# Optimization experiments

Hardware: AMD Instinct MI355X
Metric: run time of the kernel (lower is better)

## Reference

```python
import jax, jax.numpy as jnp
import numpy as np

N = 50000
E = 800000
NEG_SLOPE = 0.2


def gatv2_layer(x, src, dst, Wl, Wr, att, bias, heads, ch):
    # x: [N, Fin]; Wl/Wr: [Fin, heads*ch]; att: [heads, ch]; bias: [heads*ch]
    xl = (x @ Wl).reshape(N, heads, ch)  # source transform
    xr = (x @ Wr).reshape(N, heads, ch)  # target transform
    e = xl[src] + xr[dst]                              # [E, H, C]
    s = jnp.einsum('ehc,hc->eh', jax.nn.leaky_relu(e, NEG_SLOPE), att)  # [E, H]
    # scatter-softmax over incoming edges of each target node
    smax = jax.ops.segment_max(s, dst, num_segments=N)  # [N, H]
    ex = jnp.exp(s - smax[dst])
    denom = jax.ops.segment_sum(ex, dst, num_segments=N)
    alpha = ex / denom[dst]                             # [E, H]
    out = jax.ops.segment_sum(xl[src] * alpha[..., None], dst, num_segments=N)  # [N, H, C]
    return out.reshape(N, heads * ch) + bias


def setup_inputs() -> dict:
    key = jax.random.key(0)
    ks = jax.random.split(key, 12)
    x = jax.random.normal(ks[0], (N, 128), dtype=jnp.float32)
    edge_index = jax.random.randint(ks[1], (2, E), 0, N, dtype=jnp.int64)
    edge_attr = jax.random.normal(ks[2], (E, 16), dtype=jnp.float32)
    s1 = 1.0 / np.sqrt(128.0)
    # layer 1: 128 -> 64, heads=2 (concat -> 128)
    Wl1 = jax.random.normal(ks[3], (128, 128), dtype=jnp.float32) * s1
    Wr1 = jax.random.normal(ks[4], (128, 128), dtype=jnp.float32) * s1
    att1 = jax.random.normal(ks[5], (2, 64), dtype=jnp.float32) * 0.1
    b1 = jnp.zeros((128,), dtype=jnp.float32)
    # layer 2: 128 -> 128, heads=1
    Wl2 = jax.random.normal(ks[6], (128, 128), dtype=jnp.float32) * s1
    Wr2 = jax.random.normal(ks[7], (128, 128), dtype=jnp.float32) * s1
    att2 = jax.random.normal(ks[8], (1, 128), dtype=jnp.float32) * 0.1
    b2 = jnp.zeros((128,), dtype=jnp.float32)
    return {"x": x, "edge_index": edge_index, "edge_attr": edge_attr,
            "Wl1": Wl1, "Wr1": Wr1, "att1": att1, "b1": b1,
            "Wl2": Wl2, "Wr2": Wr2, "att2": att2, "b2": b2}


def reference(x, edge_index, edge_attr, Wl1, Wr1, att1, b1, Wl2, Wr2, att2, b2):
    # using_edge_attr=False default path: edge_attr ignored.
    # GATv2Conv default add_self_loops=True
    loops = jnp.arange(N, dtype=edge_index.dtype)
    src = jnp.concatenate([edge_index[0], loops])
    dst = jnp.concatenate([edge_index[1], loops])
    h = gatv2_layer(x, src, dst, Wl1, Wr1, att1, b1, heads=2, ch=64)
    out = gatv2_layer(h, src, dst, Wl2, Wr2, att2, b2, heads=1, ch=128)
    return out
```

## Files before the change

### kernel.cpp

```cpp
#include <hip/hip_runtime.h>

#define NEG_SLOPE 0.2f
#define NPB 256
#define CHUNK 4096
#define BCAP 5120

typedef _Float16 f16x8 __attribute__((ext_vector_type(8)));
typedef _Float16 f16x4 __attribute__((ext_vector_type(4)));
typedef _Float16 f16x2 __attribute__((ext_vector_type(2)));
typedef float    f32x4 __attribute__((ext_vector_type(4)));
typedef float    f32x8 __attribute__((ext_vector_type(8)));

#if defined(__has_builtin)
#if __has_builtin(__builtin_amdgcn_fdot2)
#define HAVE_FDOT2 1
#endif
#endif

__device__ __forceinline__ f32x8 cvt8(f16x8 v) {
    return __builtin_convertvector(v, f32x8);
}

template <int CTRL>
__device__ __forceinline__ float dpp_add(float v) {
    int o = __builtin_amdgcn_update_dpp(0, __builtin_bit_cast(int, v),
                                        CTRL, 0xF, 0xF, true);
    return v + __builtin_bit_cast(float, o);
}

__global__ __launch_bounds__(256) void prep_kernel(
    const float* __restrict__ W0, const float* __restrict__ W1,
    const float* __restrict__ W2, const float* __restrict__ W3,
    _Float16* __restrict__ wt,
    const float* __restrict__ x, _Float16* __restrict__ xh,
    _Float16* __restrict__ xlo, int total, int* __restrict__ gcursor)
{
    int t = threadIdx.x;
    if (blockIdx.x < 256) {
        if (blockIdx.x == 0) gcursor[t] = t * BCAP;
        int idx = blockIdx.x * 256 + t;
        int m = idx >> 14;
        int k = (idx >> 7) & 127;
        int n = idx & 127;
        const float* W = (m == 0) ? W0 : (m == 1) ? W1 : (m == 2) ? W2 : W3;
        wt[m * 16384 + n * 128 + k] = (_Float16)W[k * 128 + n];
    } else {
        int i = (blockIdx.x - 256) * 256 + t;
        if (i * 2 < total) {
            float2 f = *(const float2*)(x + (size_t)i * 2);
            _Float16 h0 = (_Float16)f.x, h1 = (_Float16)f.y;
            _Float16 l0 = (_Float16)(f.x - (float)h0), l1 = (_Float16)(f.y - (float)h1);
            *(f16x2*)(xh  + (size_t)i * 2) = (f16x2){h0, h1};
            *(f16x2*)(xlo + (size_t)i * 2) = (f16x2){l0, l1};
        }
    }
}

__global__ __launch_bounds__(256) void gemm_f16_kernel(
    const _Float16* __restrict__ Ahi, const _Float16* __restrict__ Alo,
    const _Float16* __restrict__ Wt0, const _Float16* __restrict__ Wt1,
    _Float16* __restrict__ Cl, _Float16* __restrict__ Cr, int N)
{
    const _Float16* Wt = blockIdx.y ? Wt1 : Wt0;
    _Float16* C = blockIdx.y ? Cr : Cl;

    __shared__ _Float16 ldsW[128 * 136];

    const int tid = threadIdx.x;
    const int wave = tid >> 6;
    const int lane = tid & 63;
    const int mrow = lane & 15;
    const int quad = lane >> 4;
    const int rbase = blockIdx.x * 128 + wave * 32;

    const int sn = tid >> 1, shf = tid & 1;
    float4 stg[8];
    {
        const float4* g = (const float4*)(Wt + sn * 128 + shf * 64);
#pragma unroll
        for (int j = 0; j < 8; j++) stg[j] = g[j];
    }

    f16x8 ah[2][4], al[2][4];
#pragma unroll
    for (int rt = 0; rt < 2; rt++) {
        int r = rbase + rt * 16 + mrow;
        if (r > N - 1) r = N - 1;
        const _Float16* pa = Ahi + (size_t)r * 128 + quad * 8;
        const _Float16* pl = Alo + (size_t)r * 128 + quad * 8;
#pragma unroll
        for (int s = 0; s < 4; s++) {
            ah[rt][s] = *(const f16x8*)(pa + s * 32);
            al[rt][s] = *(const f16x8*)(pl + s * 32);
        }
    }

    {
        float4* d = (float4*)&ldsW[sn * 136 + shf * 64];
#pragma unroll
        for (int j = 0; j < 8; j++) d[j] = stg[j];
    }

    f32x4 acc[2][8];
#pragma unroll
    for (int rt = 0; rt < 2; rt++)
#pragma unroll
        for (int c = 0; c < 8; c++) acc[rt][c] = (f32x4){0.f, 0.f, 0.f, 0.f};

    __syncthreads();

#pragma unroll
    for (int s = 0; s < 4; s++) {
#pragma unroll
        for (int c = 0; c < 8; c++) {
            f16x8 bw = *(const f16x8*)&ldsW[(c * 16 + mrow) * 136 + s * 32 + quad * 8];
            acc[0][c] = __builtin_amdgcn_mfma_f32_16x16x32_f16(ah[0][s], bw, acc[0][c], 0, 0, 0);
            acc[0][c] = __builtin_amdgcn_mfma_f32_16x16x32_f16(al[0][s], bw, acc[0][c], 0, 0, 0);
            acc[1][c] = __builtin_amdgcn_mfma_f32_16x16x32_f16(ah[1][s], bw, acc[1][c], 0, 0, 0);
            acc[1][c] = __builtin_amdgcn_mfma_f32_16x16x32_f16(al[1][s], bw, acc[1][c], 0, 0, 0);
        }
    }

#pragma unroll
    for (int rt = 0; rt < 2; rt++)
#pragma unroll
        for (int i = 0; i < 4; i++) {
            int r = rbase + rt * 16 + quad * 4 + i;
            if (r < N) {
                _Float16* cr = C + (size_t)r * 128 + mrow;
#pragma unroll
                for (int c = 0; c < 8; c++) cr[c * 16] = (_Float16)acc[rt][c][i];
            }
        }
}

__global__ __launch_bounds__(256) void bucketA_kernel(
    const int* __restrict__ ei, int* __restrict__ gcursor,
    int2* __restrict__ staging, int E)
{
    __shared__ int bh[256];
    __shared__ int bbase[256];
    int t = threadIdx.x;
    bh[t] = 0;
    __syncthreads();
    int base = blockIdx.x * CHUNK;
    int srcv[16], dstv[16], rb[16];
#pragma unroll
    for (int j = 0; j < 16; j++) {
        int e = base + t + j * 256;
        if (e < E) {
            int d = ei[E + e];
            srcv[j] = ei[e];
            dstv[j] = d;
            int bk = d >> 8;
            int r = atomicAdd(&bh[bk], 1);
            rb[j] = (r << 8) | bk;
        } else rb[j] = -1;
    }
    __syncthreads();
    if (bh[t]) bbase[t] = atomicAdd(&gcursor[t], bh[t]);
    __syncthreads();
#pragma unroll
    for (int j = 0; j < 16; j++) {
        if (rb[j] >= 0) {
            int bk = rb[j] & 255, r = rb[j] >> 8;
            staging[bbase[bk] + r] = make_int2(srcv[j], dstv[j]);
        }
    }
}

__global__ __launch_bounds__(256) void passB_kernel(
    const int2* __restrict__ staging, const int* __restrict__ gcursor,
    int* __restrict__ start, int* __restrict__ deg,
    int* __restrict__ sorted_src, int N)
{
    __shared__ int lhist[256], lscan[256], lcur[256];
    int b = blockIdx.x, t = threadIdx.x;
    int r0 = b * BCAP;
    int r1 = gcursor[b];
    lhist[t] = 0;
    __syncthreads();
    for (int i = r0 + t; i < r1; i += 256) atomicAdd(&lhist[staging[i].y & 255], 1);
    __syncthreads();
    int v = lhist[t];
    lscan[t] = v;
    __syncthreads();
    for (int off = 1; off < 256; off <<= 1) {
        int u = (t >= off) ? lscan[t - off] : 0;
        __syncthreads();
        lscan[t] += u;
        __syncthreads();
    }
    int excl = lscan[t] - v;
    int node = b * NPB + t;
    if (node < N) { start[node] = r0 + excl; deg[node] = v; }
    lcur[t] = excl;
    __syncthreads();
    for (int i = r0 + t; i < r1; i += 256) {
        int2 p = staging[i];
        int rank = atomicAdd(&lcur[p.y & 255], 1);
        sorted_src[r0 + rank] = p.x;
    }
}

template <int H, bool BFOUT>
__global__ __launch_bounds__(256) void gat_fused_kernel(
    const _Float16* __restrict__ xl, const _Float16* __restrict__ xr,
    const float* __restrict__ att, const float* __restrict__ bias,
    const int* __restrict__ start, const int* __restrict__ deg,
    const int* __restrict__ sorted_src,
    float* __restrict__ outf, _Float16* __restrict__ oh,
    _Float16* __restrict__ ol, int N)
{
    const int wid = threadIdx.x >> 6;
    const int n0 = blockIdx.x * 8 + wid * 2;
    if (n0 >= N) return;
    const bool has1 = (n0 + 1) < N;
    const int n1 = has1 ? n0 + 1 : n0;
    const int lane = threadIdx.x & 63;
    const int g  = lane >> 4;
    const int hl = lane & 15;
    const _Float16 NS = (_Float16)NEG_SLOPE;
    const float L2E = 1.44269504f;

    const f16x8 b40 = *(const f16x8*)(xr + (size_t)n0 * 128 + hl * 8);
    const f16x8 b41 = *(const f16x8*)(xr + (size_t)n1 * 128 + hl * 8);
    float4 at0 = *(const float4*)(att + hl * 8);
    float4 at1 = *(const float4*)(att + hl * 8 + 4);
#if defined(HAVE_FDOT2)
    f16x2 av0 = {(_Float16)(at0.x * L2E), (_Float16)(at0.y * L2E)};
    f16x2 av1 = {(_Float16)(at0.z * L2E), (_Float16)(at0.w * L2E)};
    f16x2 av2 = {(_Float16)(at1.x * L2E), (_Float16)(at1.y * L2E)};
    f16x2 av3 = {(_Float16)(at1.z * L2E), (_Float16)(at1.w * L2E)};
#else
    f32x8 avf = {at0.x * L2E, at0.y * L2E, at0.z * L2E, at0.w * L2E,
                 at1.x * L2E, at1.y * L2E, at1.z * L2E, at1.w * L2E};
#endif

    auto score = [&](f16x8 a_, f16x8 b4_) -> float {
        f16x8 t = a_ + b4_;
        f16x8 u = __builtin_elementwise_max(t, t * NS);
#if defined(HAVE_FDOT2)
        f16x2 u0 = __builtin_shufflevector(u, u, 0, 1);
        f16x2 u1 = __builtin_shufflevector(u, u, 2, 3);
        f16x2 u2 = __builtin_shufflevector(u, u, 4, 5);
        f16x2 u3 = __builtin_shufflevector(u, u, 6, 7);
        return __builtin_amdgcn_fdot2(u0, av0,
               __builtin_amdgcn_fdot2(u1, av1,
               __builtin_amdgcn_fdot2(u2, av2,
               __builtin_amdgcn_fdot2(u3, av3, 0.f, false), false), false), false);
#else
        f32x8 uf = cvt8(u);
        float p = 0.f;
#pragma unroll
        for (int i = 0; i < 8; i++) p += uf[i] * avf[i];
        return p;
#endif
    };

    auto red = [&](float p) -> float {
        p = dpp_add<0xB1>(p);
        p = dpp_add<0x4E>(p);
        p = dpp_add<0x141>(p);
        if (H == 1) p = dpp_add<0x140>(p);
        return p;
    };

    const int s00 = start[n0];
    const int M0  = deg[n0] + 1;
    const int s01 = start[n1];
    const int M1  = deg[n1] + 1;
    const int Mmax = (M0 > M1) ? M0 : M1;
    const int K   = (Mmax + 3) >> 2;
    const int KK  = (K + 1) & ~1;

    auto ldone = [&](int kk, int s0_, int M_, int nn) -> f16x8 {
        int iv = 4 * kk + g;
        int pos = s0_ + ((iv > 0) ? iv - 1 : 0);
        int ld = sorted_src[pos];
        int src = (iv == 0 || iv >= M_) ? nn : ld;
        return *(const f16x8*)(xl + (size_t)src * 128 + hl * 8);
    };

    f32x8 acc0 = {0.f, 0.f, 0.f, 0.f, 0.f, 0.f, 0.f, 0.f};
    f32x8 acc1 = {0.f, 0.f, 0.f, 0.f, 0.f, 0.f, 0.f, 0.f};
    float den0 = 0.f, den1 = 0.f;

    auto cone = [&](int kk, f16x8 a, f16x8 b4_, int M_, float& den_, f32x8& acc_) {
        float p = red(score(a, b4_));
        float e = (4 * kk + g < M_) ? exp2f(p) : 0.f;
        den_ += e;
#pragma unroll
        for (int i = 0; i < 8; i++)
            acc_[i] = fmaf((float)a[i], e, acc_[i]);
    };

    f16x8 c00 = ldone(0, s00, M0, n0);
    f16x8 c01 = ldone(0, s01, M1, n1);
    f16x8 c10 = ldone(1, s00, M0, n0);
    f16x8 c11 = ldone(1, s01, M1, n1);
    int k = 2;
    for (; k < KK; k += 2) {
        f16x8 d00 = ldone(k,     s00, M0, n0);
        f16x8 d01 = ldone(k,     s01, M1, n1);
        f16x8 d10 = ldone(k + 1, s00, M0, n0);
        f16x8 d11 = ldone(k + 1, s01, M1, n1);
        cone(k - 2, c00, b40, M0, den0, acc0);
        cone(k - 2, c01, b41, M1, den1, acc1);
        cone(k - 1, c10, b40, M0, den0, acc0);
        cone(k - 1, c11, b41, M1, den1, acc1);
        c00 = d00; c01 = d01; c10 = d10; c11 = d11;
    }
    cone(KK - 2, c00, b40, M0, den0, acc0);
    cone(KK - 2, c01, b41, M1, den1, acc1);
    cone(KK - 1, c10, b40, M0, den0, acc0);
    cone(KK - 1, c11, b41, M1, den1, acc1);

    den0 += __shfl_xor(den0, 16, 64);
    den0 += __shfl_xor(den0, 32, 64);
    den1 += __shfl_xor(den1, 16, 64);
    den1 += __shfl_xor(den1, 32, 64);
#pragma unroll
    for (int i = 0; i < 8; i++) {
        acc0[i] += __shfl_xor(acc0[i], 16, 64);
        acc0[i] += __shfl_xor(acc0[i], 32, 64);
        acc1[i] += __shfl_xor(acc1[i], 16, 64);
        acc1[i] += __shfl_xor(acc1[i], 32, 64);
    }

    const int which = lane >> 4;
    if (which == 0 || (which == 1 && has1)) {
        float inv = 1.0f / (which == 0 ? den0 : den1);
        int nodeo = (which == 0) ? n0 : n1;
        float4 bi0 = *(const float4*)(bias + hl * 8);
        float4 bi1 = *(const float4*)(bias + hl * 8 + 4);
        float o[8];
#pragma unroll
        for (int i = 0; i < 8; i++) {
            float a = (which == 0) ? acc0[i] : acc1[i];
            float b = (i < 4) ? ((i == 0) ? bi0.x : (i == 1) ? bi0.y : (i == 2) ? bi0.z : bi0.w)
                              : ((i == 4) ? bi1.x : (i == 5) ? bi1.y : (i == 6) ? bi1.z : bi1.w);
            o[i] = a * inv + b;
        }
        if (BFOUT) {
            f16x8 hv, lv;
#pragma unroll
            for (int i = 0; i < 8; i++) {
                _Float16 h = (_Float16)o[i];
                hv[i] = h;
                lv[i] = (_Float16)(o[i] - (float)h);
            }
            *(f16x8*)(oh + (size_t)nodeo * 128 + hl * 8) = hv;
            *(f16x8*)(ol + (size_t)nodeo * 128 + hl * 8) = lv;
        } else {
            *(float4*)(outf + (size_t)nodeo * 128 + hl * 8) =
                make_float4(o[0], o[1], o[2], o[3]);
            *(float4*)(outf + (size_t)nodeo * 128 + hl * 8 + 4) =
                make_float4(o[4], o[5], o[6], o[7]);
        }
    }
}

extern "C" void kernel_launch(void* const* d_in, const int* in_sizes, int n_in,
                              void* d_out, int out_size, void* d_ws, size_t ws_size,
                              hipStream_t stream)
{
    const float* x    = (const float*)d_in[0];
    const int*   ei   = (const int*)d_in[1];
    const float* Wl1  = (const float*)d_in[3];
    const float* Wr1  = (const float*)d_in[4];
    const float* att1 = (const float*)d_in[5];
    const float* b1   = (const float*)d_in[6];
    const float* Wl2  = (const float*)d_in[7];
    const float* Wr2  = (const float*)d_in[8];
    const float* att2 = (const float*)d_in[9];
    const float* b2   = (const float*)d_in[10];
    float* out = (float*)d_out;

    const int N  = in_sizes[0] / 128;
    const int E  = in_sizes[1] / 2;
    const int NB = (N + NPB - 1) / NPB;

    const size_t nf = (size_t)N * 128;
    _Float16* xlf  = (_Float16*)d_ws;
    _Float16* xrf  = xlf + nf;
    _Float16* ah   = xrf + nf;
    _Float16* al   = ah + nf;
    _Float16* wt   = al + nf;
    int* gcursor   = (int*)(wt + 4 * 16384);
    int* start     = gcursor + 256;
    int* deg       = start + N;
    size_t stgoff  = ((size_t)(deg + N) + 7) & ~(size_t)7;
    int2* staging  = (int2*)stgoff;
    int* sorted_src = (int*)(staging + (size_t)NB * BCAP);

    const int grid_chunk = (E + CHUNK - 1) / CHUNK;
    const int node_grid  = (N + 7) / 8;
    const int gemm_gx    = (N + 127) / 128;
    const int split_grid = (int)((nf / 2 + 255) / 256);

    prep_kernel<<<256 + split_grid, 256, 0, stream>>>(
        Wl1, Wr1, Wl2, Wr2, wt, x, ah, al, (int)nf, gcursor);

    bucketA_kernel<<<grid_chunk, 256, 0, stream>>>(ei, gcursor, staging, E);
    passB_kernel<<<NB, 256, 0, stream>>>(staging, gcursor, start, deg,
                                         sorted_src, N);

    gemm_f16_kernel<<<dim3(gemm_gx, 2), 256, 0, stream>>>(
        ah, al, wt + 0 * 16384, wt + 1 * 16384, xlf, xrf, N);
    gat_fused_kernel<2, true><<<node_grid, 256, 0, stream>>>(
        xlf, xrf, att1, b1, start, deg, sorted_src, nullptr, ah, al, N);

    gemm_f16_kernel<<<dim3(gemm_gx, 2), 256, 0, stream>>>(
        ah, al, wt + 2 * 16384, wt + 3 * 16384, xlf, xrf, N);
    gat_fused_kernel<1, false><<<node_grid, 256, 0, stream>>>(
        xlf, xrf, att2, b2, start, deg, sorted_src, out, nullptr, nullptr, N);
}
```

Measured before the change: 276.8 us.

## Merge bucketing into prep kernel and sort pass into first GEMM launch

```diff
diff --git a/kernel.cpp b/kernel.cpp
--- a/kernel.cpp
+++ b/kernel.cpp
@@ -28,24 +28,74 @@
     return v + __builtin_bit_cast(float, o);
 }
 
-__global__ __launch_bounds__(256) void prep_kernel(
+__global__ __launch_bounds__(256) void k1_prep_bucket_kernel(
     const float* __restrict__ W0, const float* __restrict__ W1,
     const float* __restrict__ W2, const float* __restrict__ W3,
     _Float16* __restrict__ wt,
     const float* __restrict__ x, _Float16* __restrict__ xh,
-    _Float16* __restrict__ xlo, int total, int* __restrict__ gcursor)
-{
+    _Float16* __restrict__ xlo, int total,
+    const int* __restrict__ ei, int* __restrict__ gcursor,
+    int2* __restrict__ staging, int E, int B0)
+{
+    __shared__ int2 pairs[CHUNK];
+    __shared__ int bh[256], bbase[256], exb[256], scn[256];
     int t = threadIdx.x;
-    if (blockIdx.x < 256) {
-        if (blockIdx.x == 0) gcursor[t] = t * BCAP;
-        int idx = blockIdx.x * 256 + t;
+    int bid = blockIdx.x;
+
+    if (bid < B0) {
+        bh[t] = 0;
+        __syncthreads();
+        int base = bid * CHUNK;
+        int srcv[16], dstv[16], rb[16];
+#pragma unroll
+        for (int j = 0; j < 16; j++) {
+            int e = base + t + j * 256;
+            if (e < E) {
+                int d = ei[E + e];
+                srcv[j] = ei[e];
+                dstv[j] = d;
+                int bk = d >> 8;
+                int r = atomicAdd(&bh[bk], 1);
+                rb[j] = (r << 8) | bk;
+            } else rb[j] = -1;
+        }
+        __syncthreads();
+        int v = bh[t];
+        scn[t] = v;
+        __syncthreads();
+        for (int off = 1; off < 256; off <<= 1) {
+            int u = (t >= off) ? scn[t - off] : 0;
+            __syncthreads();
+            scn[t] += u;
+            __syncthreads();
+        }
+        int ex = scn[t] - v;
+        int tot = scn[255];
+        exb[t] = ex;
+        if (v) bbase[t] = t * BCAP + atomicAdd(&gcursor[t], v);
+        __syncthreads();
+#pragma unroll
+        for (int j = 0; j < 16; j++) {
+            if (rb[j] >= 0) {
+                int bk = rb[j] & 255, r = rb[j] >> 8;
+                pairs[exb[bk] + r] = make_int2(srcv[j], dstv[j]);
+            }
+        }
+        __syncthreads();
+        for (int i = t; i < tot; i += 256) {
+            int2 p = pairs[i];
+            int bk = p.y >> 8;
+            staging[bbase[bk] + (i - exb[bk])] = p;
+        }
+    } else if (bid < B0 + 256) {
+        int idx = (bid - B0) * 256 + t;
         int m = idx >> 14;
         int k = (idx >> 7) & 127;
         int n = idx & 127;
         const float* W = (m == 0) ? W0 : (m == 1) ? W1 : (m == 2) ? W2 : W3;
         wt[m * 16384 + n * 128 + k] = (_Float16)W[k * 128 + n];
     } else {
-        int i = (blockIdx.x - 256) * 256 + t;
+        int i = (bid - B0 - 256) * 256 + t;
         if (i * 2 < total) {
             float2 f = *(const float2*)(x + (size_t)i * 2);
             _Float16 h0 = (_Float16)f.x, h1 = (_Float16)f.y;
@@ -56,22 +106,17 @@
     }
 }
 
-__global__ __launch_bounds__(256) void gemm_f16_kernel(
+__device__ __forceinline__ void gemm_body(
     const _Float16* __restrict__ Ahi, const _Float16* __restrict__ Alo,
-    const _Float16* __restrict__ Wt0, const _Float16* __restrict__ Wt1,
-    _Float16* __restrict__ Cl, _Float16* __restrict__ Cr, int N)
-{
-    const _Float16* Wt = blockIdx.y ? Wt1 : Wt0;
-    _Float16* C = blockIdx.y ? Cr : Cl;
-
-    __shared__ _Float16 ldsW[128 * 136];
-
+    const _Float16* __restrict__ Wt, _Float16* __restrict__ C, int N,
+    int bx, _Float16* ldsW)
+{
     const int tid = threadIdx.x;
     const int wave = tid >> 6;
     const int lane = tid & 63;
     const int mrow = lane & 15;
     const int quad = lane >> 4;
-    const int rbase = blockIdx.x * 128 + wave * 32;
+    const int rbase = bx * 128 + wave * 32;
 
     const int sn = tid >> 1, shf = tid & 1;
     float4 stg[8];
@@ -134,72 +179,61 @@
         }
 }
 
-__global__ __launch_bounds__(256) void bucketA_kernel(
-    const int* __restrict__ ei, int* __restrict__ gcursor,
-    int2* __restrict__ staging, int E)
-{
-    __shared__ int bh[256];
-    __shared__ int bbase[256];
-    int t = threadIdx.x;
-    bh[t] = 0;
-    __syncthreads();
-    int base = blockIdx.x * CHUNK;
-    int srcv[16], dstv[16], rb[16];
-#pragma unroll
-    for (int j = 0; j < 16; j++) {
-        int e = base + t + j * 256;
-        if (e < E) {
-            int d = ei[E + e];
-            srcv[j] = ei[e];
-            dstv[j] = d;
-            int bk = d >> 8;
-            int r = atomicAdd(&bh[bk], 1);
-            rb[j] = (r << 8) | bk;
-        } else rb[j] = -1;
-    }
-    __syncthreads();
-    if (bh[t]) bbase[t] = atomicAdd(&gcursor[t], bh[t]);
-    __syncthreads();
-#pragma unroll
-    for (int j = 0; j < 16; j++) {
-        if (rb[j] >= 0) {
-            int bk = rb[j] & 255, r = rb[j] >> 8;
-            staging[bbase[bk] + r] = make_int2(srcv[j], dstv[j]);
-        }
-    }
-}
-
-__global__ __launch_bounds__(256) void passB_kernel(
+__global__ __launch_bounds__(256) void gemm_f16_kernel(
+    const _Float16* __restrict__ Ahi, const _Float16* __restrict__ Alo,
+    const _Float16* __restrict__ Wt0, const _Float16* __restrict__ Wt1,
+    _Float16* __restrict__ Cl, _Float16* __restrict__ Cr, int N)
+{
+    __shared__ _Float16 ldsW[128 * 136];
+    gemm_body(Ahi, Alo, blockIdx.y ? Wt1 : Wt0, blockIdx.y ? Cr : Cl, N,
+              blockIdx.x, ldsW);
+}
+
+__global__ __launch_bounds__(256) void k2_sort_gemm_kernel(
     const int2* __restrict__ staging, const int* __restrict__ gcursor,
     int* __restrict__ start, int* __restrict__ deg,
-    int* __restrict__ sorted_src, int N)
-{
-    __shared__ int lhist[256], lscan[256], lcur[256];
-    int b = blockIdx.x, t = threadIdx.x;
-    int r0 = b * BCAP;
-    int r1 = gcursor[b];
-    lhist[t] = 0;
-    __syncthreads();
-    for (int i = r0 + t; i < r1; i += 256) atomicAdd(&lhist[staging[i].y & 255], 1);
-    __syncthreads();
-    int v = lhist[t];
-    lscan[t] = v;
-    __syncthreads();
-    for (int off = 1; off < 256; off <<= 1) {
-        int u = (t >= off) ? lscan[t - off] : 0;
-        __syncthreads();
-        lscan[t] += u;
-        __syncthreads();
-    }
-    int excl = lscan[t] - v;
-    int node = b * NPB + t;
-    if (node < N) { start[node] = r0 + excl; deg[node] = v; }
-    lcur[t] = excl;
-    __syncthreads();
-    for (int i = r0 + t; i < r1; i += 256) {
-        int2 p = staging[i];
-        int rank = atomicAdd(&lcur[p.y & 255], 1);
-        sorted_src[r0 + rank] = p.x;
+    int* __restrict__ sorted_src, int N, int NBv,
+    const _Float16* __restrict__ Ahi, const _Float16* __restrict__ Alo,
+    const _Float16* __restrict__ Wt0, const _Float16* __restrict__ Wt1,
+    _Float16* __restrict__ Cl, _Float16* __restrict__ Cr, int gx)
+{
+    __shared__ _Float16 ldsW[128 * 136];
+    int bx = blockIdx.x;
+    if (bx < NBv) {
+        int* lhist = (int*)ldsW;
+        int* lscan = lhist + 256;
+        int* lcur  = lhist + 512;
+        int b = bx, t = threadIdx.x;
+        int r0 = b * BCAP;
+        int r1 = r0 + gcursor[b];
+        lhist[t] = 0;
+        __syncthreads();
+        for (int i = r0 + t; i < r1; i += 256) atomicAdd(&lhist[staging[i].y & 255], 1);
+        __syncthreads();
+        int v = lhist[t];
+        lscan[t] = v;
+        __syncthreads();
+        for (int off = 1; off < 256; off <<= 1) {
+            int u = (t >= off) ? lscan[t - off] : 0;
+            __syncthreads();
+            lscan[t] += u;
+            __syncthreads();
+        }
+        int excl = lscan[t] - v;
+        int node = b * NPB + t;
+        if (node < N) { start[node] = r0 + excl; deg[node] = v; }
+        lcur[t] = excl;
+        __syncthreads();
+        for (int i = r0 + t; i < r1; i += 256) {
+            int2 p = staging[i];
+            int rank = atomicAdd(&lcur[p.y & 255], 1);
+            sorted_src[r0 + rank] = p.x;
+        }
+    } else {
+        int gb = bx - NBv;
+        int y = (gb >= gx) ? 1 : 0;
+        int gxi = y ? gb - gx : gb;
+        gemm_body(Ahi, Alo, y ? Wt1 : Wt0, y ? Cr : Cl, N, gxi, ldsW);
     }
 }
 
@@ -274,12 +308,13 @@
     const int K   = (Mmax + 3) >> 2;
     const int KK  = (K + 1) & ~1;
 
-    auto ldone = [&](int kk, int s0_, int M_, int nn) -> f16x8 {
+    auto gidx = [&](int kk, int s0_, int M_, int nn) -> int {
         int iv = 4 * kk + g;
-        int pos = s0_ + ((iv > 0) ? iv - 1 : 0);
-        int ld = sorted_src[pos];
-        int src = (iv == 0 || iv >= M_) ? nn : ld;
-        return *(const f16x8*)(xl + (size_t)src * 128 + hl * 8);
+        int ld = sorted_src[s0_ + ((iv > 0) ? iv - 1 : 0)];
+        return (iv == 0 || iv >= M_) ? nn : ld;
+    };
+    auto grow = [&](int s) -> f16x8 {
+        return *(const f16x8*)(xl + (size_t)s * 128 + hl * 8);
     };
 
     f32x8 acc0 = {0.f, 0.f, 0.f, 0.f, 0.f, 0.f, 0.f, 0.f};
@@ -295,26 +330,26 @@
             acc_[i] = fmaf((float)a[i], e, acc_[i]);
     };
 
-    f16x8 c00 = ldone(0, s00, M0, n0);
-    f16x8 c01 = ldone(0, s01, M1, n1);
-    f16x8 c10 = ldone(1, s00, M0, n0);
-    f16x8 c11 = ldone(1, s01, M1, n1);
-    int k = 2;
-    for (; k < KK; k += 2) {
-        f16x8 d00 = ldone(k,     s00, M0, n0);
-        f16x8 d01 = ldone(k,     s01, M1, n1);
-        f16x8 d10 = ldone(k + 1, s00, M0, n0);
-        f16x8 d11 = ldone(k + 1, s01, M1, n1);
-        cone(k - 2, c00, b40, M0, den0, acc0);
-        cone(k - 2, c01, b41, M1, den1, acc1);
-        cone(k - 1, c10, b40, M0, den0, acc0);
-        cone(k - 1, c11, b41, M1, den1, acc1);
-        c00 = d00; c01 = d01; c10 = d10; c11 = d11;
-    }
-    cone(KK - 2, c00, b40, M0, den0, acc0);
-    cone(KK - 2, c01, b41, M1, den1, acc1);
-    cone(KK - 1, c10, b40, M0, den0, acc0);
-    cone(KK - 1, c11, b41, M1, den1, acc1);
+    int i00 = gidx(0, s00, M0, n0), i01 = gidx(0, s01, M1, n1);
+    int i10 = gidx(1, s00, M0, n0), i11 = gidx(1, s01, M1, n1);
+    f16x8 r00 = grow(i00), r01 = grow(i01), r10 = grow(i10), r11 = grow(i11);
+    int j00 = gidx(2, s00, M0, n0), j01 = gidx(2, s01, M1, n1);
+    int j10 = gidx(3, s00, M0, n0), j11 = gidx(3, s01, M1, n1);
+
+    for (int k = 2; k < KK; k += 2) {
+        f16x8 t00 = grow(j00), t01 = grow(j01), t10 = grow(j10), t11 = grow(j11);
+        j00 = gidx(k + 2, s00, M0, n0); j01 = gidx(k + 2, s01, M1, n1);
+        j10 = gidx(k + 3, s00, M0, n0); j11 = gidx(k + 3, s01, M1, n1);
+        cone(k - 2, r00, b40, M0, den0, acc0);
+        cone(k - 2, r01, b41, M1, den1, acc1);
+        cone(k - 1, r10, b40, M0, den0, acc0);
+        cone(k - 1, r11, b41, M1, den1, acc1);
+        r00 = t00; r01 = t01; r10 = t10; r11 = t11;
+    }
+    cone(KK - 2, r00, b40, M0, den0, acc0);
+    cone(KK - 2, r01, b41, M1, den1, acc1);
+    cone(KK - 1, r10, b40, M0, den0, acc0);
+    cone(KK - 1, r11, b41, M1, den1, acc1);
 
     den0 += __shfl_xor(den0, 16, 64);
     den0 += __shfl_xor(den0, 32, 64);
@@ -399,15 +434,16 @@
     const int gemm_gx    = (N + 127) / 128;
     const int split_grid = (int)((nf / 2 + 255) / 256);
 
-    prep_kernel<<<256 + split_grid, 256, 0, stream>>>(
-        Wl1, Wr1, Wl2, Wr2, wt, x, ah, al, (int)nf, gcursor);
-
-    bucketA_kernel<<<grid_chunk, 256, 0, stream>>>(ei, gcursor, staging, E);
-    passB_kernel<<<NB, 256, 0, stream>>>(staging, gcursor, start, deg,
-                                         sorted_src, N);
-
-    gemm_f16_kernel<<<dim3(gemm_gx, 2), 256, 0, stream>>>(
-        ah, al, wt + 0 * 16384, wt + 1 * 16384, xlf, xrf, N);
+    hipMemsetAsync(gcursor, 0, 256 * sizeof(int), stream);
+
+    k1_prep_bucket_kernel<<<grid_chunk + 256 + split_grid, 256, 0, stream>>>(
+        Wl1, Wr1, Wl2, Wr2, wt, x, ah, al, (int)nf,
+        ei, gcursor, staging, E, grid_chunk);
+
+    k2_sort_gemm_kernel<<<NB + 2 * gemm_gx, 256, 0, stream>>>(
+        staging, gcursor, start, deg, sorted_src, N, NB,
+        ah, al, wt + 0 * 16384, wt + 1 * 16384, xlf, xrf, gemm_gx);
+
     gat_fused_kernel<2, true><<<node_grid, 256, 0, stream>>>(
         xlf, xrf, att1, b1, start, deg, sorted_src, nullptr, ah, al, N);
 
```

After: 265.2 us. 1.04x faster.
